# Kernel tuning notes

Hardware: AMD Instinct MI355X
Metric: run time of the kernel (lower is better)

The kernel has to match this reference:

```python
import jax, jax.numpy as jnp
import numpy as np

N_EMBD = 1024
N_HEAD = 16
D_HEAD = N_EMBD // N_HEAD
B, T = 4, 2048


def _layernorm(x, g, b, eps=1e-5):
    mu = jnp.mean(x, axis=-1, keepdims=True)
    var = jnp.var(x, axis=-1, keepdims=True)
    return (x - mu) * jax.lax.rsqrt(var + eps) * g + b


def setup_inputs() -> dict:
    key = jax.random.key(0)
    ks = jax.random.split(key, 16)
    C = N_EMBD
    s = 0.02
    return {
        "x": jax.random.normal(ks[0], (B, T, C), jnp.float32),
        "ln1_g": jnp.ones((C,), jnp.float32),
        "ln1_b": jnp.zeros((C,), jnp.float32),
        "Wq": jax.random.normal(ks[1], (C, C), jnp.float32) * s,
        "bq": jnp.zeros((C,), jnp.float32),
        "Wk": jax.random.normal(ks[2], (C, C), jnp.float32) * s,
        "bk": jnp.zeros((C,), jnp.float32),
        "Wv": jax.random.normal(ks[3], (C, C), jnp.float32) * s,
        "bv": jnp.zeros((C,), jnp.float32),
        "Wo": jax.random.normal(ks[4], (C, C), jnp.float32) * s,
        "bo": jnp.zeros((C,), jnp.float32),
        "ln2_g": jnp.ones((C,), jnp.float32),
        "ln2_b": jnp.zeros((C,), jnp.float32),
        "W1": jax.random.normal(ks[5], (C, 4 * C), jnp.float32) * s,
        "b1": jnp.zeros((4 * C,), jnp.float32),
        "W2": jax.random.normal(ks[6], (4 * C, C), jnp.float32) * s,
        "b2": jnp.zeros((C,), jnp.float32),
    }


def reference(x, ln1_g, ln1_b, Wq, bq, Wk, bk, Wv, bv, Wo, bo,
              ln2_g, ln2_b, W1, b1, W2, b2):
    Bx, Tx, C = x.shape
    H, D = N_HEAD, D_HEAD

    # --- attention (pre-LN) ---
    h = _layernorm(x, ln1_g, ln1_b)
    q = (h @ Wq + bq).reshape(Bx, Tx, H, D)
    k = (h @ Wk + bk).reshape(Bx, Tx, H, D)
    v = (h @ Wv + bv).reshape(Bx, Tx, H, D)
    att = jnp.einsum("bqhd,bkhd->bhqk", q, k) * (1.0 / jnp.sqrt(jnp.float32(D)))
    causal = jnp.tril(jnp.ones((Tx, Tx), bool))
    att = jnp.where(causal, att, -jnp.inf)
    att = jax.nn.softmax(att, axis=-1)
    y = jnp.einsum("bhqk,bkhd->bqhd", att, v).reshape(Bx, Tx, C)
    x = x + (y @ Wo + bo)

    # --- MLP (pre-LN), exact GELU as in torch F.gelu default ---
    h2 = _layernorm(x, ln2_g, ln2_b)
    m = jax.nn.gelu(h2 @ W1 + b1, approximate=False)
    x = x + (m @ W2 + b2)
    return x
```

## Files before the change

### kernel.cpp

```cpp
#include <hip/hip_runtime.h>
#include <hip/hip_bf16.h>
#include <math.h>

#define C_EMBD 1024
#define T_SEQ  2048
#define BATCH  4
#define NHEAD  16
#define DHEAD  64

typedef __attribute__((ext_vector_type(8))) short bf16x8;
typedef __attribute__((ext_vector_type(4))) float floatx4;

#if __has_builtin(__builtin_amdgcn_exp2f)
#define EXP2F __builtin_amdgcn_exp2f
#else
#define EXP2F exp2f
#endif

static __device__ __forceinline__ floatx4 mfma16(bf16x8 a, bf16x8 b, floatx4 c) {
    return __builtin_amdgcn_mfma_f32_16x16x32_bf16(a, b, c, 0, 0, 0);
}

static __device__ __forceinline__ void gl2lds16(const void* g, void* l) {
    __builtin_amdgcn_global_load_lds(
        (const __attribute__((address_space(1))) void*)g,
        (__attribute__((address_space(3))) void*)l, 16, 0, 0);
}

__global__ __launch_bounds__(256) void transpose_cvt(
        const float* __restrict__ W, __hip_bfloat16* __restrict__ Wt, int K, int N) {
    __shared__ float tile[32][33];
    const int tid = threadIdx.x;
    const int n0 = blockIdx.x * 32, k0 = blockIdx.y * 32;
    const int r = tid >> 3, c4 = (tid & 7) * 4;
    float4 v = *(const float4*)&W[(size_t)(k0 + r) * N + n0 + c4];
    tile[r][c4 + 0] = v.x; tile[r][c4 + 1] = v.y;
    tile[r][c4 + 2] = v.z; tile[r][c4 + 3] = v.w;
    __syncthreads();
    __align__(8) __hip_bfloat16 ob[4];
    ob[0] = __float2bfloat16(tile[c4 + 0][r]);
    ob[1] = __float2bfloat16(tile[c4 + 1][r]);
    ob[2] = __float2bfloat16(tile[c4 + 2][r]);
    ob[3] = __float2bfloat16(tile[c4 + 3][r]);
    *(short4*)&Wt[(size_t)(n0 + r) * K + k0 + c4] = *(short4*)ob;
}

__global__ __launch_bounds__(256) void transpose_cvt4(
        const float* __restrict__ W0, const float* __restrict__ W1_,
        const float* __restrict__ W2_, const float* __restrict__ W3_,
        __hip_bfloat16* __restrict__ T0, __hip_bfloat16* __restrict__ T1,
        __hip_bfloat16* __restrict__ T2, __hip_bfloat16* __restrict__ T3) {
    __shared__ float tile[32][33];
    const float* W = (blockIdx.z == 0) ? W0 : (blockIdx.z == 1) ? W1_ :
                     (blockIdx.z == 2) ? W2_ : W3_;
    __hip_bfloat16* Wt = (blockIdx.z == 0) ? T0 : (blockIdx.z == 1) ? T1 :
                         (blockIdx.z == 2) ? T2 : T3;
    const int tid = threadIdx.x;
    const int n0 = blockIdx.x * 32, k0 = blockIdx.y * 32;
    const int r = tid >> 3, c4 = (tid & 7) * 4;
    float4 v = *(const float4*)&W[(size_t)(k0 + r) * 1024 + n0 + c4];
    tile[r][c4 + 0] = v.x; tile[r][c4 + 1] = v.y;
    tile[r][c4 + 2] = v.z; tile[r][c4 + 3] = v.w;
    __syncthreads();
    __align__(8) __hip_bfloat16 ob[4];
    ob[0] = __float2bfloat16(tile[c4 + 0][r]);
    ob[1] = __float2bfloat16(tile[c4 + 1][r]);
    ob[2] = __float2bfloat16(tile[c4 + 2][r]);
    ob[3] = __float2bfloat16(tile[c4 + 3][r]);
    *(short4*)&Wt[(size_t)(n0 + r) * 1024 + k0 + c4] = *(short4*)ob;
}

__global__ __launch_bounds__(256) void ln_bf16(
        const float* __restrict__ x, const float* __restrict__ g,
        const float* __restrict__ b, __hip_bfloat16* __restrict__ out) {
    const int row = blockIdx.x, tid = threadIdx.x;
    const float4 v = ((const float4*)(x + (size_t)row * C_EMBD))[tid];
    float s  = v.x + v.y + v.z + v.w;
    float sq = v.x * v.x + v.y * v.y + v.z * v.z + v.w * v.w;
    #pragma unroll
    for (int off = 1; off < 64; off <<= 1) {
        s  += __shfl_xor(s, off);
        sq += __shfl_xor(sq, off);
    }
    __shared__ float ps[4], pq[4];
    if ((tid & 63) == 0) { ps[tid >> 6] = s; pq[tid >> 6] = sq; }
    __syncthreads();
    s  = ps[0] + ps[1] + ps[2] + ps[3];
    sq = pq[0] + pq[1] + pq[2] + pq[3];
    const float mu   = s * (1.0f / C_EMBD);
    const float var  = sq * (1.0f / C_EMBD) - mu * mu;
    const float rstd = rsqrtf(var + 1e-5f);
    const float4 gv = ((const float4*)g)[tid];
    const float4 bv = ((const float4*)b)[tid];
    __align__(8) __hip_bfloat16 ob[4];
    ob[0] = __float2bfloat16((v.x - mu) * rstd * gv.x + bv.x);
    ob[1] = __float2bfloat16((v.y - mu) * rstd * gv.y + bv.y);
    ob[2] = __float2bfloat16((v.z - mu) * rstd * gv.z + bv.z);
    ob[3] = __float2bfloat16((v.w - mu) * rstd * gv.w + bv.w);
    *(short4*)&out[(size_t)row * C_EMBD + tid * 4] = *(short4*)ob;
}

template <int EP>
__global__ __launch_bounds__(256, 2) void gemm_bt(
        const __hip_bfloat16* __restrict__ A, const __hip_bfloat16* __restrict__ Bt,
        int M, int N, int K,
        const float* __restrict__ ba, const float* __restrict__ bb, const float* __restrict__ bc,
        __hip_bfloat16* __restrict__ o0, __hip_bfloat16* __restrict__ o1,
        __hip_bfloat16* __restrict__ o2, float* __restrict__ of,
        const float* __restrict__ resid) {
    __shared__ __align__(16) __hip_bfloat16 As[2][128 * 32];
    __shared__ __align__(16) __hip_bfloat16 Bs[2][128 * 32];
    const int tid  = threadIdx.x;

    const int gx  = gridDim.x;
    const int nwg = gx * gridDim.y;
    const int lin = blockIdx.x + gx * blockIdx.y;
    const int cpx = nwg >> 3;
    const int wg  = (lin & 7) * cpx + (lin >> 3);
    const int by  = (wg & 7) + 8 * (wg / (gx << 3));
    const int bx  = (wg >> 3) % gx;
    const int n0  = bx * 128;
    const int m0  = by * 128;

    const int wave = tid >> 6, lane = tid & 63;
    const int l15  = lane & 15, quad = lane >> 4;
    const int wm   = (wave & 1) * 64, wn = (wave >> 1) * 64;
    const int c0   = wave * 2;
    const int sr   = lane >> 2;
    const int sc   = (lane & 3) * 8;

    const floatx4 z4 = {0.f, 0.f, 0.f, 0.f};
    floatx4 acc[4][4];
    #pragma unroll
    for (int i = 0; i < 4; i++)
        #pragma unroll
        for (int j = 0; j < 4; j++) acc[i][j] = z4;

    auto stage = [&](const int buf, const int k0) {
        gl2lds16(&A [(m0 + c0 * 16 + sr) * K + k0 + sc],       &As[buf][c0 * 512]);
        gl2lds16(&A [(m0 + (c0 + 1) * 16 + sr) * K + k0 + sc], &As[buf][(c0 + 1) * 512]);
        gl2lds16(&Bt[(n0 + c0 * 16 + sr) * K + k0 + sc],       &Bs[buf][c0 * 512]);
        gl2lds16(&Bt[(n0 + (c0 + 1) * 16 + sr) * K + k0 + sc], &Bs[buf][(c0 + 1) * 512]);
    };

    stage(0, 0);
    const int nk = K >> 5;
    for (int t = 0; t < nk; ++t) {
        const int cur = t & 1;
        if (t + 1 < nk) {
            stage(cur ^ 1, (t + 1) * 32);
            asm volatile("s_waitcnt vmcnt(4)" ::: "memory");
        } else {
            asm volatile("s_waitcnt vmcnt(0)" ::: "memory");
        }
        __builtin_amdgcn_s_barrier();
        asm volatile("" ::: "memory");
        bf16x8 af[4], bfr[4];
        #pragma unroll
        for (int i = 0; i < 4; i++)
            af[i] = *(const bf16x8*)&As[cur][(wm + i * 16 + l15) * 32 + quad * 8];
        #pragma unroll
        for (int j = 0; j < 4; j++)
            bfr[j] = *(const bf16x8*)&Bs[cur][(wn + j * 16 + l15) * 32 + quad * 8];
        #pragma unroll
        for (int i = 0; i < 4; i++)
            #pragma unroll
            for (int j = 0; j < 4; j++)
                acc[i][j] = mfma16(af[i], bfr[j], acc[i][j]);
        asm volatile("" ::: "memory");
        __builtin_amdgcn_s_barrier();
    }

    #pragma unroll
    for (int i = 0; i < 4; i++) {
        #pragma unroll
        for (int j = 0; j < 4; j++) {
            const int col = n0 + wn + j * 16 + l15;
            #pragma unroll
            for (int r = 0; r < 4; r++) {
                const int m = m0 + wm + i * 16 + quad * 4 + r;
                float val = acc[i][j][r];
                if (EP == 1) {
                    val += ba[col];
                    of[m * N + col] = resid[m * N + col] + val;
                } else {
                    val += ba[col];
                    of[m * N + col] += val;
                }
            }
        }
    }
}

template <int EP>
__global__ __launch_bounds__(512, 2) void gemm256_8ph(
        const __hip_bfloat16* __restrict__ A, const __hip_bfloat16* __restrict__ Bt,
        int M, int N, int K,
        const float* __restrict__ ba, const float* __restrict__ bb, const float* __restrict__ bc,
        __hip_bfloat16* __restrict__ o0, __hip_bfloat16* __restrict__ o1,
        __hip_bfloat16* __restrict__ o2) {
    __shared__ __align__(16) __hip_bfloat16 As[2][256 * 64];
    __shared__ __align__(16) __hip_bfloat16 Bs[2][256 * 64];
    const int tid = threadIdx.x;

    const int gx  = gridDim.x;
    const int nwg = gx * gridDim.y;
    const int lin = blockIdx.x + gx * blockIdx.y;
    const int cpx = nwg >> 3;
    const int wg  = (lin & 7) * cpx + (lin >> 3);
    const int by  = (wg & 7) + 8 * (wg / (gx << 3));
    const int bx  = (wg >> 3) % gx;
    const int n0  = bx * 256;
    const int m0  = by * 256;

    const int wave = tid >> 6, lane = tid & 63;
    const int l15 = lane & 15, quad = lane >> 4;
    const int wr  = wave >> 2, wc = wave & 3;
    const int swz = l15 & 7;
    const int sr8 = tid >> 3;
    const int sg  = (tid & 7) ^ (sr8 & 7);

    const floatx4 z4 = {0.f, 0.f, 0.f, 0.f};
    floatx4 acc[8][4];
    #pragma unroll
    for (int i = 0; i < 8; i++)
        #pragma unroll
        for (int j = 0; j < 4; j++) acc[i][j] = z4;

    auto stA = [&](const int buf, const int half, const int k0) {
        #pragma unroll
        for (int s = 0; s < 2; s++) {
            const int r0 = half * 128 + s * 64;
            gl2lds16(&A[(size_t)(m0 + r0 + sr8) * K + k0 + sg * 8],
                     &As[buf][r0 * 64 + wave * 512]);
        }
    };
    auto stB = [&](const int buf, const int half, const int k0) {
        #pragma unroll
        for (int s = 0; s < 2; s++) {
            const int r0 = half * 128 + s * 64;
            gl2lds16(&Bt[(size_t)(n0 + r0 + sr8) * K + k0 + sg * 8],
                     &Bs[buf][r0 * 64 + wave * 512]);
        }
    };
    auto ldA = [&](const int buf, const int mi, const int ks) -> bf16x8 {
        return *(const bf16x8*)&As[buf][(mi * 32 + wr * 16 + l15) * 64 +
                                        (((ks * 4 + quad) ^ swz) * 8)];
    };
    auto ldB = [&](const int buf, const int nj, const int ks) -> bf16x8 {
        return *(const bf16x8*)&Bs[buf][(wc * 64 + nj * 16 + l15) * 64 +
                                        (((ks * 4 + quad) ^ swz) * 8)];
    };

    const int NT = K >> 6;
    stA(0, 0, 0); stB(0, 0, 0); stA(0, 1, 0); stB(0, 1, 0);
    stA(1, 0, 64); stB(1, 0, 64);
    asm volatile("s_waitcnt vmcnt(4)" ::: "memory");
    __builtin_amdgcn_s_barrier();
    asm volatile("" ::: "memory");

    for (int t = 0; t < NT; ++t) {
        const int cur = t & 1;
        const int kn1 = (t + 1) * 64, kn2 = (t + 2) * 64;
        const bool s1 = (t + 1 < NT), s2 = (t + 2 < NT);
        bf16x8 bfrag[4][2];
        #pragma unroll
        for (int p = 0; p < 4; ++p) {
            bf16x8 afr[2][2];
            if (p == 0) {
                #pragma unroll
                for (int nj = 0; nj < 4; nj++)
                    #pragma unroll
                    for (int ks = 0; ks < 2; ks++)
                        bfrag[nj][ks] = ldB(cur, nj, ks);
            }
            #pragma unroll
            for (int i = 0; i < 2; i++)
                #pragma unroll
                for (int ks = 0; ks < 2; ks++)
                    afr[i][ks] = ldA(cur, 2 * p + i, ks);
            if (p == 0)      { if (s1) stA(cur ^ 1, 1, kn1); }
            else if (p == 1) { if (s1) stB(cur ^ 1, 1, kn1); }
            else if (p == 2) { if (s2) stA(cur, 0, kn2); }
            else             { if (s2) stB(cur, 0, kn2); }
            asm volatile("" ::: "memory");
            __builtin_amdgcn_s_barrier();
            asm volatile("s_waitcnt lgkmcnt(0)" ::: "memory");
            __builtin_amdgcn_s_setprio(1);
            #pragma unroll
            for (int i = 0; i < 2; i++)
                #pragma unroll
                for (int nj = 0; nj < 4; nj++)
                    #pragma unroll
                    for (int ks = 0; ks < 2; ks++)
                        acc[2 * p + i][nj] = mfma16(afr[i][ks], bfrag[nj][ks], acc[2 * p + i][nj]);
            __builtin_amdgcn_s_setprio(0);
            if (p == 3) {
                if (s2) { asm volatile("s_waitcnt vmcnt(4)" ::: "memory"); }
                else    { asm volatile("s_waitcnt vmcnt(0)" ::: "memory"); }
            }
            asm volatile("" ::: "memory");
            __builtin_amdgcn_s_barrier();
            asm volatile("" ::: "memory");
        }
    }

    __hip_bfloat16* slab = (wc < 2) ? (&As[0][0] + wc * 16384)
                                    : (&Bs[0][0] + (wc - 2) * 16384);
    const int lid = wr * 64 + lane;

    if (EP == 0) {
        const int which = n0 >> 10;
        const int cn0   = (n0 & 1023) + wc * 64;
        const int head  = cn0 >> 6;
        const int bidx  = m0 >> 11;
        const int t0    = m0 & 2047;
        const float* bp = (which == 0) ? ba : (which == 1) ? bb : bc;
        float bias[4];
        #pragma unroll
        for (int nj = 0; nj < 4; nj++) bias[nj] = bp[cn0 + nj * 16 + l15];
        if (which < 2) {
            const float scale = (which == 0) ? 0.18033688011112042f : 1.0f;
            #pragma unroll
            for (int mi = 0; mi < 8; mi++)
                #pragma unroll
                for (int nj = 0; nj < 4; nj++)
                    #pragma unroll
                    for (int r = 0; r < 4; r++) {
                        const int row = mi * 32 + wr * 16 + quad * 4 + r;
                        slab[row * 64 + nj * 16 + l15] =
                            __float2bfloat16((acc[mi][nj][r] + bias[nj]) * scale);
                    }
            __syncthreads();
            __hip_bfloat16* dst = ((which == 0) ? o0 : o1) +
                ((size_t)(bidx * NHEAD + head) * T_SEQ + t0) * DHEAD;
            #pragma unroll
            for (int s = 0; s < 16; s++)
                *(bf16x8*)&dst[s * 1024 + lid * 8] = *(const bf16x8*)&slab[s * 1024 + lid * 8];
        } else {
            #pragma unroll
            for (int mi = 0; mi < 8; mi++)
                #pragma unroll
                for (int nj = 0; nj < 4; nj++) {
                    const int d   = nj * 16 + l15;
                    const int key = (d & 7) << 3;
                    #pragma unroll
                    for (int r = 0; r < 4; r++) {
                        const int row = mi * 32 + wr * 16 + quad * 4 + r;
                        slab[d * 256 + (row ^ key)] =
                            __float2bfloat16(acc[mi][nj][r] + bias[nj]);
                    }
                }
            __syncthreads();
            __hip_bfloat16* dst = o2 + (size_t)(bidx * NHEAD + head) * DHEAD * T_SEQ + t0;
            const int dly = lid >> 5;
            const int tly = (lid & 31) * 8;
            #pragma unroll
            for (int s = 0; s < 16; s++) {
                const int d = s * 4 + dly;
                *(bf16x8*)&dst[(size_t)d * T_SEQ + tly] =
                    *(const bf16x8*)&slab[d * 256 + (tly ^ ((d & 7) << 3))];
            }
        }
    } else {
        float bias[4];
        #pragma unroll
        for (int nj = 0; nj < 4; nj++) bias[nj] = ba[n0 + wc * 64 + nj * 16 + l15];
        #pragma unroll
        for (int mi = 0; mi < 8; mi++)
            #pragma unroll
            for (int nj = 0; nj < 4; nj++)
                #pragma unroll
                for (int r = 0; r < 4; r++) {
                    const int row = mi * 32 + wr * 16 + quad * 4 + r;
                    const float val = acc[mi][nj][r] + bias[nj];
                    const float gl = 0.5f * val * (1.0f + erff(val * 0.70710678118654752f));
                    slab[row * 64 + nj * 16 + l15] = __float2bfloat16(gl);
                }
        __syncthreads();
        #pragma unroll
        for (int s = 0; s < 16; s++) {
            const int row = s * 16 + (lid >> 3);
            *(bf16x8*)&o0[(size_t)(m0 + row) * N + n0 + wc * 64 + (lid & 7) * 8] =
                *(const bf16x8*)&slab[row * 64 + (lid & 7) * 8];
        }
    }
}

__global__ __launch_bounds__(256, 2) void attn_fa(
        const __hip_bfloat16* __restrict__ q, const __hip_bfloat16* __restrict__ k,
        const __hip_bfloat16* __restrict__ vt, __hip_bfloat16* __restrict__ y) {
    __shared__ __align__(16) __hip_bfloat16 Ks[2][64 * 64];
    __shared__ __align__(16) __hip_bfloat16 Vs[2][64 * 64];
    __shared__ __align__(16) __hip_bfloat16 pl[4][32 * 72];
    const int tid = threadIdx.x;
    const int wave = tid >> 6, lane = tid & 63;
    const int l15 = lane & 15, quad = lane >> 4;
    const int sw  = l15 & 7;
    const int lr  = lane >> 3;
    const int gsw = (lane & 7) ^ lr;

    const int lin  = blockIdx.x;
    const int xcd  = lin & 7;
    const int slot = lin >> 3;
    const int bh   = xcd * 8 + (slot >> 3);
    const int jA   = slot & 7;

    const __hip_bfloat16* qp = q + (size_t)bh * T_SEQ * DHEAD;
    const __hip_bfloat16* kp = k + (size_t)bh * T_SEQ * DHEAD;
    const __hip_bfloat16* vp = vt + (size_t)bh * DHEAD * T_SEQ;
    __hip_bfloat16* myp = &pl[wave][0];
    const int b = bh >> 4, head = bh & 15;
    const floatx4 z4 = {0.f, 0.f, 0.f, 0.f};

    auto stage = [&](const int buf, const int kb) {
        #pragma unroll
        for (int j = 0; j < 2; j++) {
            const int rb = wave * 16 + j * 8;
            gl2lds16(&kp[(size_t)(kb + rb + lr) * DHEAD + gsw * 8], &Ks[buf][rb * 64]);
            gl2lds16(&vp[(size_t)(rb + lr) * T_SEQ + kb + gsw * 8], &Vs[buf][rb * 64]);
        }
    };

    auto segment = [&](const int tile) {
        const int q0 = tile * 128;
        const int qw = q0 + wave * 32;
        const int cc = tile * 2 + 1;

        bf16x8 bq[2][2];
        #pragma unroll
        for (int qi = 0; qi < 2; qi++)
            #pragma unroll
            for (int h = 0; h < 2; h++)
                bq[qi][h] = *(const bf16x8*)&qp[(qw + qi * 16 + l15) * DHEAD + h * 32 + quad * 8];

        floatx4 oac[2][4];
        #pragma unroll
        for (int qi = 0; qi < 2; qi++)
            #pragma unroll
            for (int nd = 0; nd < 4; nd++) oac[qi][nd] = z4;
        float li[2] = {0.f, 0.f};

        stage(0, 0);

        for (int t = 0; t <= cc; t++) {
            const int cur = t & 1;
            if (t < cc) {
                stage(cur ^ 1, (t + 1) * 64);
                asm volatile("s_waitcnt vmcnt(4)" ::: "memory");
            } else {
                asm volatile("s_waitcnt vmcnt(0)" ::: "memory");
            }
            __builtin_amdgcn_s_barrier();
            asm volatile("" ::: "memory");

            const int kb = t * 64;
            const bool act = (kb <= qw + 31);
            if (act) {
                const bool dg = (kb + 63 > qw);
                bf16x8 kf[4][2];
                #pragma unroll
                for (int nt = 0; nt < 4; nt++)
                    #pragma unroll
                    for (int h = 0; h < 2; h++)
                        kf[nt][h] = *(const bf16x8*)&Ks[cur][(nt * 16 + l15) * 64 + (((h * 4 + quad) ^ sw) * 8)];
                floatx4 sa[2][4];
                #pragma unroll
                for (int qi = 0; qi < 2; qi++)
                    #pragma unroll
                    for (int nt = 0; nt < 4; nt++) sa[qi][nt] = z4;
                #pragma unroll
                for (int nt = 0; nt < 4; nt++)
                    #pragma unroll
                    for (int h = 0; h < 2; h++) {
                        sa[0][nt] = mfma16(kf[nt][h], bq[0][h], sa[0][nt]);
                        sa[1][nt] = mfma16(kf[nt][h], bq[1][h], sa[1][nt]);
                    }
                if (dg) {
                    #pragma unroll
                    for (int qi = 0; qi < 2; qi++)
                        #pragma unroll
                        for (int nt = 0; nt < 4; nt++)
                            #pragma unroll
                            for (int r = 0; r < 4; r++)
                                if (kb + nt * 16 + quad * 4 + r > qw + qi * 16 + l15)
                                    sa[qi][nt][r] = -INFINITY;
                }
                #pragma unroll
                for (int qi = 0; qi < 2; qi++) {
                    float sm = 0.f;
                    #pragma unroll
                    for (int nt = 0; nt < 4; nt++) {
                        __align__(8) __hip_bfloat16 pk[4];
                        #pragma unroll
                        for (int r = 0; r < 4; r++) {
                            const float p = EXP2F(sa[qi][nt][r]);
                            sm += p;
                            pk[r] = __float2bfloat16(p);
                        }
                        *(short4*)&myp[(qi * 16 + l15) * 72 + nt * 16 + quad * 4] = *(short4*)pk;
                    }
                    li[qi] += sm;
                }
                bf16x8 vf[4][2];
                #pragma unroll
                for (int nd = 0; nd < 4; nd++)
                    #pragma unroll
                    for (int kh = 0; kh < 2; kh++)
                        vf[nd][kh] = *(const bf16x8*)&Vs[cur][(nd * 16 + l15) * 64 + (((kh * 4 + quad) ^ sw) * 8)];
                asm volatile("s_waitcnt lgkmcnt(0)" ::: "memory");
                bf16x8 pf[2][2];
                #pragma unroll
                for (int qi = 0; qi < 2; qi++)
                    #pragma unroll
                    for (int kh = 0; kh < 2; kh++)
                        pf[qi][kh] = *(const bf16x8*)&myp[(qi * 16 + l15) * 72 + kh * 32 + quad * 8];
                #pragma unroll
                for (int nd = 0; nd < 4; nd++)
                    #pragma unroll
                    for (int kh = 0; kh < 2; kh++) {
                        oac[0][nd] = mfma16(vf[nd][kh], pf[0][kh], oac[0][nd]);
                        oac[1][nd] = mfma16(vf[nd][kh], pf[1][kh], oac[1][nd]);
                    }
            }
            asm volatile("" ::: "memory");
            __builtin_amdgcn_s_barrier();
        }

        float inv[2];
        #pragma unroll
        for (int qi = 0; qi < 2; qi++) {
            float l = li[qi];
            l += __shfl_xor(l, 16);
            l += __shfl_xor(l, 32);
            inv[qi] = 1.0f / l;
        }
        #pragma unroll
        for (int qi = 0; qi < 2; qi++)
            #pragma unroll
            for (int nd = 0; nd < 4; nd++) {
                __align__(8) __hip_bfloat16 ok[4];
                #pragma unroll
                for (int r = 0; r < 4; r++) ok[r] = __float2bfloat16(oac[qi][nd][r] * inv[qi]);
                *(short4*)&myp[(qi * 16 + l15) * 72 + nd * 16 + quad * 4] = *(short4*)ok;
            }
        asm volatile("s_waitcnt lgkmcnt(0)" ::: "memory");
        #pragma unroll
        for (int half = 0; half < 2; half++) {
            const int row = half * 16 + (lane >> 2);
            const int cb  = (lane & 3) * 16;
            const bf16x8 v0 = *(const bf16x8*)&myp[row * 72 + cb];
            const bf16x8 v1 = *(const bf16x8*)&myp[row * 72 + cb + 8];
            __hip_bfloat16* yr = &y[(size_t)(b * T_SEQ + qw + row) * C_EMBD + head * DHEAD + cb];
            *(bf16x8*)yr       = v0;
            *(bf16x8*)(yr + 8) = v1;
        }
        asm volatile("s_waitcnt vmcnt(0)" ::: "memory");
    };

    segment(jA);
    segment(15 - jA);
}

extern "C" void kernel_launch(void* const* d_in, const int* in_sizes, int n_in,
                              void* d_out, int out_size, void* d_ws, size_t ws_size,
                              hipStream_t stream) {
    const float* x     = (const float*)d_in[0];
    const float* ln1_g = (const float*)d_in[1];
    const float* ln1_b = (const float*)d_in[2];
    const float* Wq    = (const float*)d_in[3];
    const float* bq    = (const float*)d_in[4];
    const float* Wk    = (const float*)d_in[5];
    const float* bk    = (const float*)d_in[6];
    const float* Wv    = (const float*)d_in[7];
    const float* bv    = (const float*)d_in[8];
    const float* Wo    = (const float*)d_in[9];
    const float* bo    = (const float*)d_in[10];
    const float* ln2_g = (const float*)d_in[11];
    const float* ln2_b = (const float*)d_in[12];
    const float* W1    = (const float*)d_in[13];
    const float* b1    = (const float*)d_in[14];
    const float* W2    = (const float*)d_in[15];
    const float* b2    = (const float*)d_in[16];
    float* out = (float*)d_out;

    char* ws = (char*)d_ws;
    __hip_bfloat16* wqkvt = (__hip_bfloat16*)(ws);
    __hip_bfloat16* wot   = (__hip_bfloat16*)(ws + 6291456);
    __hip_bfloat16* w1t   = (__hip_bfloat16*)(ws + 8388608);
    __hip_bfloat16* w2t   = (__hip_bfloat16*)(ws + 16777216);
    __hip_bfloat16* hbuf  = (__hip_bfloat16*)(ws + 25165824);
    __hip_bfloat16* qbuf  = (__hip_bfloat16*)(ws + 41943040);
    __hip_bfloat16* kbuf  = (__hip_bfloat16*)(ws + 58720256);
    __hip_bfloat16* vbuf  = (__hip_bfloat16*)(ws + 75497472);
    __hip_bfloat16* ybuf  = (__hip_bfloat16*)(ws + 92274688);
    __hip_bfloat16* mbuf  = (__hip_bfloat16*)(ws + 41943040);

    transpose_cvt4<<<dim3(32, 32, 4), 256, 0, stream>>>(
        Wq, Wk, Wv, Wo, wqkvt, wqkvt + 1024 * 1024, wqkvt + 2048 * 1024, wot);
    transpose_cvt<<<dim3(128, 32), 256, 0, stream>>>(W1, w1t, 1024, 4096);
    transpose_cvt<<<dim3(32, 128), 256, 0, stream>>>(W2, w2t, 4096, 1024);

    ln_bf16<<<8192, 256, 0, stream>>>(x, ln1_g, ln1_b, hbuf);

    gemm256_8ph<0><<<dim3(12, 32), 512, 0, stream>>>(hbuf, wqkvt, 8192, 3072, 1024,
        bq, bk, bv, qbuf, kbuf, vbuf);

    attn_fa<<<dim3(512), 256, 0, stream>>>(qbuf, kbuf, vbuf, ybuf);

    gemm_bt<1><<<dim3(8, 64), 256, 0, stream>>>(ybuf, wot, 8192, 1024, 1024,
        bo, nullptr, nullptr, nullptr, nullptr, nullptr, out, x);

    ln_bf16<<<8192, 256, 0, stream>>>(out, ln2_g, ln2_b, hbuf);

    gemm256_8ph<2><<<dim3(16, 32), 512, 0, stream>>>(hbuf, w1t, 8192, 4096, 1024,
        b1, nullptr, nullptr, mbuf, nullptr, nullptr);

    gemm_bt<3><<<dim3(8, 64), 256, 0, stream>>>(mbuf, w2t, 8192, 1024, 4096,
        b2, nullptr, nullptr, nullptr, nullptr, nullptr, out, nullptr);
}
```

Measured before the change: 513.9 us.

## Replace 128x128 output-projection/MLP-down GEMM with 256x128 eight-phase pipelined kernel

```diff
diff --git a/kernel.cpp b/kernel.cpp
--- a/kernel.cpp
+++ b/kernel.cpp
@@ -101,16 +101,13 @@
 }
 
 template <int EP>
-__global__ __launch_bounds__(256, 2) void gemm_bt(
+__global__ __launch_bounds__(512, 2) void gemm_n128_8ph(
         const __hip_bfloat16* __restrict__ A, const __hip_bfloat16* __restrict__ Bt,
-        int M, int N, int K,
-        const float* __restrict__ ba, const float* __restrict__ bb, const float* __restrict__ bc,
-        __hip_bfloat16* __restrict__ o0, __hip_bfloat16* __restrict__ o1,
-        __hip_bfloat16* __restrict__ o2, float* __restrict__ of,
-        const float* __restrict__ resid) {
-    __shared__ __align__(16) __hip_bfloat16 As[2][128 * 32];
-    __shared__ __align__(16) __hip_bfloat16 Bs[2][128 * 32];
-    const int tid  = threadIdx.x;
+        int M, int N, int K, const float* __restrict__ ba,
+        float* __restrict__ of, const float* __restrict__ resid) {
+    __shared__ __align__(16) __hip_bfloat16 As[2][256 * 64];
+    __shared__ __align__(16) __hip_bfloat16 Bs[2][128 * 64];
+    const int tid = threadIdx.x;
 
     const int gx  = gridDim.x;
     const int nwg = gx * gridDim.y;
@@ -120,14 +117,14 @@
     const int by  = (wg & 7) + 8 * (wg / (gx << 3));
     const int bx  = (wg >> 3) % gx;
     const int n0  = bx * 128;
-    const int m0  = by * 128;
+    const int m0  = by * 256;
 
     const int wave = tid >> 6, lane = tid & 63;
-    const int l15  = lane & 15, quad = lane >> 4;
-    const int wm   = (wave & 1) * 64, wn = (wave >> 1) * 64;
-    const int c0   = wave * 2;
-    const int sr   = lane >> 2;
-    const int sc   = (lane & 3) * 8;
+    const int l15 = lane & 15, quad = lane >> 4;
+    const int wr  = wave >> 1, wc = wave & 1;
+    const int swz = l15 & 7;
+    const int sr8 = tid >> 3;
+    const int sg  = (tid & 7) ^ (sr8 & 7);
 
     const floatx4 z4 = {0.f, 0.f, 0.f, 0.f};
     floatx4 acc[4][4];
@@ -136,56 +133,93 @@
         #pragma unroll
         for (int j = 0; j < 4; j++) acc[i][j] = z4;
 
-    auto stage = [&](const int buf, const int k0) {
-        gl2lds16(&A [(m0 + c0 * 16 + sr) * K + k0 + sc],       &As[buf][c0 * 512]);
-        gl2lds16(&A [(m0 + (c0 + 1) * 16 + sr) * K + k0 + sc], &As[buf][(c0 + 1) * 512]);
-        gl2lds16(&Bt[(n0 + c0 * 16 + sr) * K + k0 + sc],       &Bs[buf][c0 * 512]);
-        gl2lds16(&Bt[(n0 + (c0 + 1) * 16 + sr) * K + k0 + sc], &Bs[buf][(c0 + 1) * 512]);
-    };
-
-    stage(0, 0);
-    const int nk = K >> 5;
-    for (int t = 0; t < nk; ++t) {
+    auto stA = [&](const int buf, const int half, const int k0) {
+        #pragma unroll
+        for (int s = 0; s < 2; s++) {
+            const int r0 = half * 128 + s * 64;
+            gl2lds16(&A[(size_t)(m0 + r0 + sr8) * K + k0 + sg * 8],
+                     &As[buf][r0 * 64 + wave * 512]);
+        }
+    };
+    auto stB = [&](const int buf, const int k0) {
+        #pragma unroll
+        for (int s = 0; s < 2; s++) {
+            const int r0 = s * 64;
+            gl2lds16(&Bt[(size_t)(n0 + r0 + sr8) * K + k0 + sg * 8],
+                     &Bs[buf][r0 * 64 + wave * 512]);
+        }
+    };
+    auto ldA = [&](const int buf, const int mi, const int ks) -> bf16x8 {
+        return *(const bf16x8*)&As[buf][(mi * 64 + wr * 16 + l15) * 64 +
+                                        (((ks * 4 + quad) ^ swz) * 8)];
+    };
+    auto ldB = [&](const int buf, const int nj, const int ks) -> bf16x8 {
+        return *(const bf16x8*)&Bs[buf][(wc * 64 + nj * 16 + l15) * 64 +
+                                        (((ks * 4 + quad) ^ swz) * 8)];
+    };
+
+    const int NT = K >> 6;
+    stA(0, 0, 0); stA(0, 1, 0); stB(0, 0);
+    stA(1, 0, 64);
+    asm volatile("s_waitcnt vmcnt(2)" ::: "memory");
+    __builtin_amdgcn_s_barrier();
+    asm volatile("" ::: "memory");
+
+    for (int t = 0; t < NT; ++t) {
         const int cur = t & 1;
-        if (t + 1 < nk) {
-            stage(cur ^ 1, (t + 1) * 32);
-            asm volatile("s_waitcnt vmcnt(4)" ::: "memory");
-        } else {
-            asm volatile("s_waitcnt vmcnt(0)" ::: "memory");
-        }
-        __builtin_amdgcn_s_barrier();
-        asm volatile("" ::: "memory");
-        bf16x8 af[4], bfr[4];
-        #pragma unroll
-        for (int i = 0; i < 4; i++)
-            af[i] = *(const bf16x8*)&As[cur][(wm + i * 16 + l15) * 32 + quad * 8];
-        #pragma unroll
-        for (int j = 0; j < 4; j++)
-            bfr[j] = *(const bf16x8*)&Bs[cur][(wn + j * 16 + l15) * 32 + quad * 8];
-        #pragma unroll
-        for (int i = 0; i < 4; i++)
-            #pragma unroll
-            for (int j = 0; j < 4; j++)
-                acc[i][j] = mfma16(af[i], bfr[j], acc[i][j]);
-        asm volatile("" ::: "memory");
-        __builtin_amdgcn_s_barrier();
+        const int kn1 = (t + 1) * 64, kn2 = (t + 2) * 64;
+        const bool s1 = (t + 1 < NT), s2 = (t + 2 < NT);
+        bf16x8 bfrag[4][2];
+        #pragma unroll
+        for (int p = 0; p < 4; ++p) {
+            bf16x8 afr[2];
+            if (p == 0) {
+                #pragma unroll
+                for (int nj = 0; nj < 4; nj++)
+                    #pragma unroll
+                    for (int ks = 0; ks < 2; ks++)
+                        bfrag[nj][ks] = ldB(cur, nj, ks);
+            }
+            #pragma unroll
+            for (int ks = 0; ks < 2; ks++)
+                afr[ks] = ldA(cur, p, ks);
+            if (p == 0)      { if (s1) stA(cur ^ 1, 1, kn1); }
+            else if (p == 1) { if (s1) stB(cur ^ 1, kn1); }
+            else if (p == 2) { if (s2) stA(cur, 0, kn2); }
+            asm volatile("" ::: "memory");
+            __builtin_amdgcn_s_barrier();
+            asm volatile("s_waitcnt lgkmcnt(0)" ::: "memory");
+            __builtin_amdgcn_s_setprio(1);
+            #pragma unroll
+            for (int nj = 0; nj < 4; nj++)
+                #pragma unroll
+                for (int ks = 0; ks < 2; ks++)
+                    acc[p][nj] = mfma16(afr[ks], bfrag[nj][ks], acc[p][nj]);
+            __builtin_amdgcn_s_setprio(0);
+            if (p == 3) {
+                if (s2) { asm volatile("s_waitcnt vmcnt(2)" ::: "memory"); }
+                else    { asm volatile("s_waitcnt vmcnt(0)" ::: "memory"); }
+            }
+            asm volatile("" ::: "memory");
+            __builtin_amdgcn_s_barrier();
+            asm volatile("" ::: "memory");
+        }
     }
 
     #pragma unroll
-    for (int i = 0; i < 4; i++) {
-        #pragma unroll
-        for (int j = 0; j < 4; j++) {
-            const int col = n0 + wn + j * 16 + l15;
+    for (int mi = 0; mi < 4; mi++) {
+        #pragma unroll
+        for (int nj = 0; nj < 4; nj++) {
+            const int col = n0 + wc * 64 + nj * 16 + l15;
+            const float bias = ba[col];
             #pragma unroll
             for (int r = 0; r < 4; r++) {
-                const int m = m0 + wm + i * 16 + quad * 4 + r;
-                float val = acc[i][j][r];
+                const int m = m0 + mi * 64 + wr * 16 + quad * 4 + r;
+                const float val = acc[mi][nj][r] + bias;
                 if (EP == 1) {
-                    val += ba[col];
-                    of[m * N + col] = resid[m * N + col] + val;
+                    of[(size_t)m * N + col] = resid[(size_t)m * N + col] + val;
                 } else {
-                    val += ba[col];
-                    of[m * N + col] += val;
+                    of[(size_t)m * N + col] += val;
                 }
             }
         }
@@ -608,14 +642,14 @@
 
     attn_fa<<<dim3(512), 256, 0, stream>>>(qbuf, kbuf, vbuf, ybuf);
 
-    gemm_bt<1><<<dim3(8, 64), 256, 0, stream>>>(ybuf, wot, 8192, 1024, 1024,
-        bo, nullptr, nullptr, nullptr, nullptr, nullptr, out, x);
+    gemm_n128_8ph<1><<<dim3(8, 32), 512, 0, stream>>>(ybuf, wot, 8192, 1024, 1024,
+        bo, out, x);
 
     ln_bf16<<<8192, 256, 0, stream>>>(out, ln2_g, ln2_b, hbuf);
 
     gemm256_8ph<2><<<dim3(16, 32), 512, 0, stream>>>(hbuf, w1t, 8192, 4096, 1024,
         b1, nullptr, nullptr, mbuf, nullptr, nullptr);
 
-    gemm_bt<3><<<dim3(8, 64), 256, 0, stream>>>(mbuf, w2t, 8192, 1024, 4096,
-        b2, nullptr, nullptr, nullptr, nullptr, nullptr, out, nullptr);
-}
+    gemm_n128_8ph<3><<<dim3(8, 32), 512, 0, stream>>>(mbuf, w2t, 8192, 1024, 4096,
+        b2, out, nullptr);
+}
```

After: 518.4 us. No clear change (+0.9%).
